# Performance work log

Measured on AMD Instinct MI355X. Metric: run time of the kernel, lower is better.

## Reference

```python
import jax, jax.numpy as jnp
import numpy as np

N, E, F, UNITS, K = 50000, 500000, 128, 256, 3


def setup_inputs() -> dict:
    key = jax.random.key(0)
    k1, k2, k3 = jax.random.split(key, 3)
    x = jax.random.normal(k1, (N, F), dtype=jnp.float32)
    edge_index = jax.random.randint(k2, (2, E), 0, N)
    edge_weight = jnp.ones((E,), dtype=jnp.float32)
    kernel = jax.random.normal(k3, (F * (K + 1), UNITS), dtype=jnp.float32) * 0.02
    bias = jnp.zeros((UNITS,), dtype=jnp.float32)
    return {"x": x, "edge_index": edge_index, "edge_weight": edge_weight,
            "kernel": kernel, "bias": bias}


def _gcn_norm_edge(edge_index, edge_weight, num_nodes):
    # renorm=False, improved=False (tf_geometric gcn_norm_edge):
    # symmetric-normalize original edges, THEN append self-loops with weight 1.0
    row, col = edge_index[0], edge_index[1]
    deg = jax.ops.segment_sum(edge_weight, row, num_segments=num_nodes)
    deg_inv_sqrt = jnp.where(deg > 0, 1.0 / jnp.sqrt(jnp.maximum(deg, 1e-12)), 0.0)
    w = deg_inv_sqrt[row] * edge_weight * deg_inv_sqrt[col]
    loop = jnp.arange(num_nodes)
    row = jnp.concatenate([row, loop])
    col = jnp.concatenate([col, loop])
    w = jnp.concatenate([w, jnp.ones((num_nodes,), dtype=w.dtype)])
    return row, col, w


def reference(x, edge_index, edge_weight, kernel, bias):
    n = x.shape[0]
    row, col, w = _gcn_norm_edge(edge_index, edge_weight, n)
    xs = [x]
    for _ in range(K):
        # out[col] += x[row] * w  (gather -> weight -> scatter-sum)
        h = jax.ops.segment_sum(xs[-1][row] * w[:, None], col, num_segments=n)
        xs.append(h)
    h = jnp.concatenate(xs, axis=-1)  # [N, F*(K+1)]
    out = h @ kernel + bias           # [N, UNITS]
    return out
```

## Files before the change

### kernel.cpp

```cpp
#include <hip/hip_runtime.h>

constexpr int NN = 50000;
constexpr int EE = 500000;
constexpr int FF = 128;
constexpr int UU = 256;
constexpr int KK = 512;
constexpr int NB = (NN + 255) / 256;

using bf16x8 = __attribute__((ext_vector_type(8))) short;
using f32x4  = __attribute__((ext_vector_type(4))) float;

__device__ inline float bf2f(unsigned short b) {
    unsigned u = (unsigned)b << 16; float f; __builtin_memcpy(&f, &u, 4); return f;
}
__device__ inline unsigned short f2bf(float f) {
    unsigned u; __builtin_memcpy(&u, &f, 4);
    u = u + 0x7fffu + ((u >> 16) & 1u);
    return (unsigned short)(u >> 16);
}

typedef __attribute__((address_space(1))) const void GASV;
typedef __attribute__((address_space(3))) void LASV;
__device__ inline void gload_lds16(const void* g, void* l) {
    __builtin_amdgcn_global_load_lds((GASV*)g, (LASV*)l, 16, 0, 0);
}


__global__ __launch_bounds__(256) void k_degcnt(const int* __restrict__ row,
                                                const int* __restrict__ col,
                                                const float* __restrict__ ew,
                                                float* __restrict__ deg,
                                                int* __restrict__ cnt, int E) {
    int e = blockIdx.x * 256 + threadIdx.x;
    if (e < E) {
        atomicAdd(&deg[row[e]], ew[e]);
        atomicAdd(&cnt[col[e]], 1);
    }
}


__global__ __launch_bounds__(256) void k_scan1(const int* __restrict__ cnt,
                                               int* __restrict__ offs,
                                               int* __restrict__ bsum,
                                               float* __restrict__ deg) {
    const int t = threadIdx.x;
    const int gid = blockIdx.x * 256 + t;
    if (gid < NN) {
        float d = deg[gid];
        deg[gid] = (d > 0.f) ? (1.0f / sqrtf(fmaxf(d, 1e-12f))) : 0.f;
    }
    int v = (gid < NN) ? cnt[gid] : 0;
    __shared__ int ts[256];
    ts[t] = v; __syncthreads();
    for (int d = 1; d < 256; d <<= 1) {
        int a = ts[t]; int b = (t >= d) ? ts[t - d] : 0;
        __syncthreads(); ts[t] = a + b; __syncthreads();
    }
    if (gid < NN) offs[gid] = ts[t] - v;
    if (t == 255) bsum[blockIdx.x] = ts[255];
}

__global__ __launch_bounds__(256) void k_scan2(int* __restrict__ bsum) {
    const int t = threadIdx.x;
    int v = (t < NB) ? bsum[t] : 0;
    __shared__ int ts[256];
    ts[t] = v; __syncthreads();
    for (int d = 1; d < 256; d <<= 1) {
        int a = ts[t]; int b = (t >= d) ? ts[t - d] : 0;
        __syncthreads(); ts[t] = a + b; __syncthreads();
    }
    if (t < NB) bsum[t] = ts[t] - v;
}

__global__ __launch_bounds__(256) void k_scan3(int* __restrict__ offs,
                                               int* __restrict__ cursor,
                                               const int* __restrict__ bsum) {
    const int gid = blockIdx.x * 256 + threadIdx.x;
    if (gid < NN) {
        int val = offs[gid] + bsum[blockIdx.x];
        offs[gid] = val;
        cursor[gid] = val;
    }
    if (gid == 0) offs[NN] = EE;
}


__global__ __launch_bounds__(256) void k_scatter(const int* __restrict__ row,
                                                 const int* __restrict__ col,
                                                 const float* __restrict__ ew,
                                                 const float* __restrict__ dis,
                                                 int* __restrict__ cursor,
                                                 int* __restrict__ rows_s,
                                                 float* __restrict__ w_s, int E) {
    int e = blockIdx.x * 256 + threadIdx.x;
    if (e < E) {
        int r = row[e], c = col[e];
        int slot = atomicAdd(&cursor[c], 1);
        rows_s[slot] = r;
        w_s[slot] = dis[r] * ew[e] * dis[c];
    }
}


__global__ __launch_bounds__(256) void k_xcast(const float4* __restrict__ x4,
                                               unsigned short* __restrict__ H) {
    int i = blockIdx.x * 256 + threadIdx.x;
    if (i < NN * 32) {
        int n = i >> 5, c4 = i & 31;
        float4 v = x4[i];
        ushort4 o;
        o.x = f2bf(v.x); o.y = f2bf(v.y); o.z = f2bf(v.z); o.w = f2bf(v.w);
        *reinterpret_cast<ushort4*>(H + (size_t)n * KK + c4 * 4) = o;
    }
}

__global__ __launch_bounds__(256) void k_wcast(const float* __restrict__ W,
                                               unsigned short* __restrict__ Wt) {
    int t = blockIdx.x * 256 + threadIdx.x;
    if (t < KK * UU) {
        int k = t >> 8, c = t & 255;
        Wt[(size_t)c * KK + k] = f2bf(W[t]);
    }
}


__global__ __launch_bounds__(256) void k_prop(const int* __restrict__ offs,
                                              const int* __restrict__ rows_s,
                                              const float* __restrict__ w_s,
                                              unsigned short* __restrict__ H,
                                              int sin, int sout) {
    int wid = (blockIdx.x * 256 + threadIdx.x) >> 6;
    int lane = threadIdx.x & 63;
    if (wid >= NN) return;
    const unsigned short* bin = H + (size_t)sin * FF;
    unsigned self = *reinterpret_cast<const unsigned*>(bin + (size_t)wid * KK + lane * 2);
    float a0 = bf2f((unsigned short)self);
    float a1 = bf2f((unsigned short)(self >> 16));
    const int beg = offs[wid], end = offs[wid + 1];
    int e = beg;
    for (; e + 4 <= end; e += 4) {
        int r0 = rows_s[e], r1 = rows_s[e + 1], r2 = rows_s[e + 2], r3 = rows_s[e + 3];
        float w0 = w_s[e], w1 = w_s[e + 1], w2 = w_s[e + 2], w3 = w_s[e + 3];
        unsigned v0 = *reinterpret_cast<const unsigned*>(bin + (size_t)r0 * KK + lane * 2);
        unsigned v1 = *reinterpret_cast<const unsigned*>(bin + (size_t)r1 * KK + lane * 2);
        unsigned v2 = *reinterpret_cast<const unsigned*>(bin + (size_t)r2 * KK + lane * 2);
        unsigned v3 = *reinterpret_cast<const unsigned*>(bin + (size_t)r3 * KK + lane * 2);
        a0 += bf2f((unsigned short)v0) * w0 + bf2f((unsigned short)v1) * w1
            + bf2f((unsigned short)v2) * w2 + bf2f((unsigned short)v3) * w3;
        a1 += bf2f((unsigned short)(v0 >> 16)) * w0 + bf2f((unsigned short)(v1 >> 16)) * w1
            + bf2f((unsigned short)(v2 >> 16)) * w2 + bf2f((unsigned short)(v3 >> 16)) * w3;
    }
    for (; e < end; ++e) {
        int r = rows_s[e];
        float wv = w_s[e];
        unsigned v = *reinterpret_cast<const unsigned*>(bin + (size_t)r * KK + lane * 2);
        a0 += bf2f((unsigned short)v) * wv;
        a1 += bf2f((unsigned short)(v >> 16)) * wv;
    }
    unsigned o = (unsigned)f2bf(a0) | ((unsigned)f2bf(a1) << 16);
    *reinterpret_cast<unsigned*>(H + (size_t)sout * FF + (size_t)wid * KK + lane * 2) = o;
}


__global__ __launch_bounds__(256, 2) void k_gemm(const unsigned short* __restrict__ H,
                                                 const unsigned short* __restrict__ Wt,
                                                 const float* __restrict__ bias,
                                                 float* __restrict__ out) {
    __shared__ __align__(16) char As[2][128 * 128];
    __shared__ __align__(16) char Bs[2][128 * 128];
    const int t = threadIdx.x;
    const int lane = t & 63;
    const int wv = t >> 6;
    const int wm = wv >> 1;
    const int wn = wv & 1;
    const int brow = (blockIdx.x >> 1) * 128;
    const int bcol = (blockIdx.x & 1) * 128;

    const int r8  = lane >> 3;
    const int b16 = (lane & 7) * 16;

    f32x4 acc[4][4] = {};

    auto stage = [&](int buf, int ks) {
#pragma unroll
        for (int i = 0; i < 8; ++i) {
            int c = wv * 8 + i;
            if (c < 16) {
                int r = c * 8 + r8;
                int gr = brow + r; if (gr >= NN) gr = NN - 1;
                const char* src = (const char*)H + (size_t)gr * (KK * 2) + ks * 128
                                  + (b16 ^ ((r & 7) << 4));
                gload_lds16(src, &As[buf][c * 1024]);
            } else {
                int cc = (c - 16) * 8 + r8;
                int gc = bcol + cc;
                const char* src = (const char*)Wt + (size_t)gc * (KK * 2) + ks * 128
                                  + (b16 ^ ((cc & 7) << 4));
                gload_lds16(src, &Bs[buf][(c - 16) * 1024]);
            }
        }
    };

    auto compute = [&](int buf) {
        bf16x8 af[2][4], bfr[2][4];
#pragma unroll
        for (int kk = 0; kk < 2; ++kk) {
#pragma unroll
            for (int f = 0; f < 4; ++f) {
                int r = wm * 64 + f * 16 + (lane & 15);
                int ba = (kk * 64 + (lane >> 4) * 16) ^ ((r & 7) << 4);
                af[kk][f] = *reinterpret_cast<const bf16x8*>(&As[buf][r * 128 + ba]);
                int cc = wn * 64 + f * 16 + (lane & 15);
                int bb = (kk * 64 + (lane >> 4) * 16) ^ ((cc & 7) << 4);
                bfr[kk][f] = *reinterpret_cast<const bf16x8*>(&Bs[buf][cc * 128 + bb]);
            }
        }
#pragma unroll
        for (int kk = 0; kk < 2; ++kk)
#pragma unroll
            for (int fm = 0; fm < 4; ++fm)
#pragma unroll
                for (int fn = 0; fn < 4; ++fn)
                    acc[fm][fn] = __builtin_amdgcn_mfma_f32_16x16x32_bf16(
                        af[kk][fm], bfr[kk][fn], acc[fm][fn], 0, 0, 0);
    };

    stage(0, 0);
    __syncthreads();
    for (int ks = 0; ks < 8; ++ks) {
        if (ks < 7) stage((ks + 1) & 1, ks + 1);
        compute(ks & 1);
        __syncthreads();
    }

#pragma unroll
    for (int fn = 0; fn < 4; ++fn) {
        int col = bcol + wn * 64 + fn * 16 + (lane & 15);
        float bs = bias[col];
#pragma unroll
        for (int fm = 0; fm < 4; ++fm) {
#pragma unroll
            for (int r4 = 0; r4 < 4; ++r4) {
                int grow = brow + wm * 64 + fm * 16 + (lane >> 4) * 4 + r4;
                if (grow < NN)
                    out[(size_t)grow * UU + col] = acc[fm][fn][r4] + bs;
            }
        }
    }
}


extern "C" void kernel_launch(void* const* d_in, const int* in_sizes, int n_in,
                              void* d_out, int out_size, void* d_ws, size_t ws_size,
                              hipStream_t stream) {
    const float* x    = (const float*)d_in[0];
    const int*   ei   = (const int*)d_in[1];
    const float* ew   = (const float*)d_in[2];
    const float* Wk   = (const float*)d_in[3];
    const float* bias = (const float*)d_in[4];
    float* out = (float*)d_out;

    const int* row = ei;
    const int* col = ei + EE;

    char* ws = (char*)d_ws;
    size_t off = 0;
    auto alloc = [&](size_t bytes) {
        size_t o = off;
        off += (bytes + 255) & ~(size_t)255;
        return o;
    };
    float*          deg    = (float*)(ws + alloc((size_t)NN * sizeof(float)));
    int*            cnt    = (int*)  (ws + alloc((size_t)NN * sizeof(int)));
    int*            cursor = (int*)  (ws + alloc((size_t)NN * sizeof(int)));
    int*            offs   = (int*)  (ws + alloc((size_t)(NN + 1) * sizeof(int)));
    int*            bsum   = (int*)  (ws + alloc((size_t)256 * sizeof(int)));
    int*            rows_s = (int*)  (ws + alloc((size_t)EE * sizeof(int)));
    float*          w_s    = (float*)(ws + alloc((size_t)EE * sizeof(float)));
    unsigned short* Hcat   = (unsigned short*)(ws + alloc((size_t)NN * KK * sizeof(short)));
    unsigned short* Wt     = (unsigned short*)(ws + alloc((size_t)KK * UU * sizeof(short)));

    const int geb = (EE + 255) / 256;

    hipMemsetAsync(deg, 0, (size_t)NN * sizeof(float), stream);
    hipMemsetAsync(cnt, 0, (size_t)NN * sizeof(int), stream);
    k_degcnt<<<geb, 256, 0, stream>>>(row, col, ew, deg, cnt, EE);
    k_scan1<<<NB, 256, 0, stream>>>(cnt, offs, bsum, deg);
    k_scan2<<<1, 256, 0, stream>>>(bsum);
    k_scan3<<<NB, 256, 0, stream>>>(offs, cursor, bsum);
    k_scatter<<<geb, 256, 0, stream>>>(row, col, ew, deg, cursor, rows_s, w_s, EE);

    k_xcast<<<(NN * 32 + 255) / 256, 256, 0, stream>>>((const float4*)x, Hcat);
    k_wcast<<<(KK * UU + 255) / 256, 256, 0, stream>>>(Wk, Wt);

    const int gprop = (NN * 64 + 255) / 256;
    k_prop<<<gprop, 256, 0, stream>>>(offs, rows_s, w_s, Hcat, 0, 1);
    k_prop<<<gprop, 256, 0, stream>>>(offs, rows_s, w_s, Hcat, 1, 2);
    k_prop<<<gprop, 256, 0, stream>>>(offs, rows_s, w_s, Hcat, 2, 3);

    k_gemm<<<391 * 2, 256, 0, stream>>>(Hcat, Wt, bias, out);
}
```

Before: 303.3 us.

## Fuse setup kernels, pack edge data, and split wavefront across edges in propagation

Folds the x-to-bf16 cast into the degree/count kernel and the weight transpose-cast into the scatter kernel, which cuts the launch count. Packs each edge's row index and normalized weight into one uint2, so propagation does a single 8-byte load per edge. Propagation now splits each wavefront into four groups of 16 lanes; each group handles a different edge with 16-byte feature loads, and the partial sums are combined with cross-lane shuffles. This gives more memory-level parallelism per wavefront, at the cost of extra shuffles and more register pressure.

```diff
diff --git a/kernel.cpp b/kernel.cpp
--- a/kernel.cpp
+++ b/kernel.cpp
@@ -26,15 +26,27 @@
 }
 
 
-__global__ __launch_bounds__(256) void k_degcnt(const int* __restrict__ row,
-                                                const int* __restrict__ col,
-                                                const float* __restrict__ ew,
-                                                float* __restrict__ deg,
-                                                int* __restrict__ cnt, int E) {
-    int e = blockIdx.x * 256 + threadIdx.x;
-    if (e < E) {
-        atomicAdd(&deg[row[e]], ew[e]);
-        atomicAdd(&cnt[col[e]], 1);
+__global__ __launch_bounds__(256) void k_deg_x(const int* __restrict__ row,
+                                               const int* __restrict__ col,
+                                               const float* __restrict__ ew,
+                                               float* __restrict__ deg,
+                                               int* __restrict__ cnt,
+                                               const float4* __restrict__ x4,
+                                               unsigned short* __restrict__ H) {
+    const int i = blockIdx.x * 256 + threadIdx.x;
+    if (i < NN * 32) {
+        int n = i >> 5, c4 = i & 31;
+        float4 v = x4[i];
+        ushort4 o;
+        o.x = f2bf(v.x); o.y = f2bf(v.y); o.z = f2bf(v.z); o.w = f2bf(v.w);
+        *reinterpret_cast<ushort4*>(H + (size_t)n * KK + c4 * 4) = o;
+    }
+    if (blockIdx.x % 3 == 0) {
+        int e = (blockIdx.x / 3) * 256 + threadIdx.x;
+        if (e < EE) {
+            atomicAdd(&deg[row[e]], ew[e]);
+            atomicAdd(&cnt[col[e]], 1);
+        }
     }
 }
 
@@ -90,75 +102,85 @@
                                                  const float* __restrict__ ew,
                                                  const float* __restrict__ dis,
                                                  int* __restrict__ cursor,
-                                                 int* __restrict__ rows_s,
-                                                 float* __restrict__ w_s, int E) {
-    int e = blockIdx.x * 256 + threadIdx.x;
-    if (e < E) {
+                                                 uint2* __restrict__ edata,
+                                                 const float* __restrict__ W,
+                                                 unsigned short* __restrict__ Wt) {
+    const int e = blockIdx.x * 256 + threadIdx.x;
+    if (e < EE) {
         int r = row[e], c = col[e];
         int slot = atomicAdd(&cursor[c], 1);
-        rows_s[slot] = r;
-        w_s[slot] = dis[r] * ew[e] * dis[c];
-    }
-}
-
-
-__global__ __launch_bounds__(256) void k_xcast(const float4* __restrict__ x4,
-                                               unsigned short* __restrict__ H) {
-    int i = blockIdx.x * 256 + threadIdx.x;
-    if (i < NN * 32) {
-        int n = i >> 5, c4 = i & 31;
-        float4 v = x4[i];
-        ushort4 o;
-        o.x = f2bf(v.x); o.y = f2bf(v.y); o.z = f2bf(v.z); o.w = f2bf(v.w);
-        *reinterpret_cast<ushort4*>(H + (size_t)n * KK + c4 * 4) = o;
-    }
-}
-
-__global__ __launch_bounds__(256) void k_wcast(const float* __restrict__ W,
-                                               unsigned short* __restrict__ Wt) {
-    int t = blockIdx.x * 256 + threadIdx.x;
-    if (t < KK * UU) {
-        int k = t >> 8, c = t & 255;
-        Wt[(size_t)c * KK + k] = f2bf(W[t]);
+        float wv = dis[r] * ew[e] * dis[c];
+        uint2 d; d.x = (unsigned)r; __builtin_memcpy(&d.y, &wv, 4);
+        edata[slot] = d;
+    }
+    if (e < KK * UU) {
+        int k = e >> 8, c = e & 255;
+        Wt[(size_t)c * KK + k] = f2bf(W[e]);
     }
 }
 
 
 __global__ __launch_bounds__(256) void k_prop(const int* __restrict__ offs,
-                                              const int* __restrict__ rows_s,
-                                              const float* __restrict__ w_s,
+                                              const uint2* __restrict__ edata,
                                               unsigned short* __restrict__ H,
                                               int sin, int sout) {
-    int wid = (blockIdx.x * 256 + threadIdx.x) >> 6;
-    int lane = threadIdx.x & 63;
-    if (wid >= NN) return;
+    const int wid = (blockIdx.x * 256 + threadIdx.x) >> 6;
+    const int lane = threadIdx.x & 63;
+    const int g = lane >> 4;
+    const int sl = lane & 15;
+
     const unsigned short* bin = H + (size_t)sin * FF;
-    unsigned self = *reinterpret_cast<const unsigned*>(bin + (size_t)wid * KK + lane * 2);
-    float a0 = bf2f((unsigned short)self);
-    float a1 = bf2f((unsigned short)(self >> 16));
+    const unsigned short* rowp = bin + (size_t)wid * KK + sl * 8;
+
+    float a[8];
+    {
+        uint4 s4 = *reinterpret_cast<const uint4*>(rowp);
+        const unsigned sw[4] = {s4.x, s4.y, s4.z, s4.w};
+#pragma unroll
+        for (int j = 0; j < 8; ++j) {
+            float v = bf2f((unsigned short)(sw[j >> 1] >> ((j & 1) * 16)));
+            a[j] = (g == 0) ? v : 0.f;
+        }
+    }
+
     const int beg = offs[wid], end = offs[wid + 1];
-    int e = beg;
-    for (; e + 4 <= end; e += 4) {
-        int r0 = rows_s[e], r1 = rows_s[e + 1], r2 = rows_s[e + 2], r3 = rows_s[e + 3];
-        float w0 = w_s[e], w1 = w_s[e + 1], w2 = w_s[e + 2], w3 = w_s[e + 3];
-        unsigned v0 = *reinterpret_cast<const unsigned*>(bin + (size_t)r0 * KK + lane * 2);
-        unsigned v1 = *reinterpret_cast<const unsigned*>(bin + (size_t)r1 * KK + lane * 2);
-        unsigned v2 = *reinterpret_cast<const unsigned*>(bin + (size_t)r2 * KK + lane * 2);
-        unsigned v3 = *reinterpret_cast<const unsigned*>(bin + (size_t)r3 * KK + lane * 2);
-        a0 += bf2f((unsigned short)v0) * w0 + bf2f((unsigned short)v1) * w1
-            + bf2f((unsigned short)v2) * w2 + bf2f((unsigned short)v3) * w3;
-        a1 += bf2f((unsigned short)(v0 >> 16)) * w0 + bf2f((unsigned short)(v1 >> 16)) * w1
-            + bf2f((unsigned short)(v2 >> 16)) * w2 + bf2f((unsigned short)(v3 >> 16)) * w3;
-    }
-    for (; e < end; ++e) {
-        int r = rows_s[e];
-        float wv = w_s[e];
-        unsigned v = *reinterpret_cast<const unsigned*>(bin + (size_t)r * KK + lane * 2);
-        a0 += bf2f((unsigned short)v) * wv;
-        a1 += bf2f((unsigned short)(v >> 16)) * wv;
-    }
-    unsigned o = (unsigned)f2bf(a0) | ((unsigned)f2bf(a1) << 16);
-    *reinterpret_cast<unsigned*>(H + (size_t)sout * FF + (size_t)wid * KK + lane * 2) = o;
+    int e = beg + g;
+    for (; e + 4 < end; e += 8) {
+        uint2 d0 = edata[e], d1 = edata[e + 4];
+        float w0, w1; __builtin_memcpy(&w0, &d0.y, 4); __builtin_memcpy(&w1, &d1.y, 4);
+        uint4 v0 = *reinterpret_cast<const uint4*>(bin + (size_t)d0.x * KK + sl * 8);
+        uint4 v1 = *reinterpret_cast<const uint4*>(bin + (size_t)d1.x * KK + sl * 8);
+        const unsigned u0[4] = {v0.x, v0.y, v0.z, v0.w};
+        const unsigned u1[4] = {v1.x, v1.y, v1.z, v1.w};
+#pragma unroll
+        for (int j = 0; j < 8; ++j)
+            a[j] += bf2f((unsigned short)(u0[j >> 1] >> ((j & 1) * 16))) * w0
+                  + bf2f((unsigned short)(u1[j >> 1] >> ((j & 1) * 16))) * w1;
+    }
+    if (e < end) {
+        uint2 d0 = edata[e];
+        float w0; __builtin_memcpy(&w0, &d0.y, 4);
+        uint4 v0 = *reinterpret_cast<const uint4*>(bin + (size_t)d0.x * KK + sl * 8);
+        const unsigned u0[4] = {v0.x, v0.y, v0.z, v0.w};
+#pragma unroll
+        for (int j = 0; j < 8; ++j)
+            a[j] += bf2f((unsigned short)(u0[j >> 1] >> ((j & 1) * 16))) * w0;
+    }
+
+#pragma unroll
+    for (int j = 0; j < 8; ++j) {
+        a[j] += __shfl_xor(a[j], 16);
+        a[j] += __shfl_xor(a[j], 32);
+    }
+
+    if (lane < 16) {
+        uint4 o;
+        o.x = (unsigned)f2bf(a[0]) | ((unsigned)f2bf(a[1]) << 16);
+        o.y = (unsigned)f2bf(a[2]) | ((unsigned)f2bf(a[3]) << 16);
+        o.z = (unsigned)f2bf(a[4]) | ((unsigned)f2bf(a[5]) << 16);
+        o.w = (unsigned)f2bf(a[6]) | ((unsigned)f2bf(a[7]) << 16);
+        *reinterpret_cast<uint4*>(H + (size_t)sout * FF + (size_t)wid * KK + sl * 8) = o;
+    }
 }
 
 
@@ -275,28 +297,25 @@
     int*            cursor = (int*)  (ws + alloc((size_t)NN * sizeof(int)));
     int*            offs   = (int*)  (ws + alloc((size_t)(NN + 1) * sizeof(int)));
     int*            bsum   = (int*)  (ws + alloc((size_t)256 * sizeof(int)));
-    int*            rows_s = (int*)  (ws + alloc((size_t)EE * sizeof(int)));
-    float*          w_s    = (float*)(ws + alloc((size_t)EE * sizeof(float)));
+    uint2*          edata  = (uint2*)(ws + alloc((size_t)EE * sizeof(uint2)));
     unsigned short* Hcat   = (unsigned short*)(ws + alloc((size_t)NN * KK * sizeof(short)));
     unsigned short* Wt     = (unsigned short*)(ws + alloc((size_t)KK * UU * sizeof(short)));
 
-    const int geb = (EE + 255) / 256;
-
     hipMemsetAsync(deg, 0, (size_t)NN * sizeof(float), stream);
     hipMemsetAsync(cnt, 0, (size_t)NN * sizeof(int), stream);
-    k_degcnt<<<geb, 256, 0, stream>>>(row, col, ew, deg, cnt, EE);
+
+    k_deg_x<<<(NN * 32 + 255) / 256, 256, 0, stream>>>(row, col, ew, deg, cnt,
+                                                       (const float4*)x, Hcat);
     k_scan1<<<NB, 256, 0, stream>>>(cnt, offs, bsum, deg);
     k_scan2<<<1, 256, 0, stream>>>(bsum);
     k_scan3<<<NB, 256, 0, stream>>>(offs, cursor, bsum);
-    k_scatter<<<geb, 256, 0, stream>>>(row, col, ew, deg, cursor, rows_s, w_s, EE);
-
-    k_xcast<<<(NN * 32 + 255) / 256, 256, 0, stream>>>((const float4*)x, Hcat);
-    k_wcast<<<(KK * UU + 255) / 256, 256, 0, stream>>>(Wk, Wt);
-
-    const int gprop = (NN * 64 + 255) / 256;
-    k_prop<<<gprop, 256, 0, stream>>>(offs, rows_s, w_s, Hcat, 0, 1);
-    k_prop<<<gprop, 256, 0, stream>>>(offs, rows_s, w_s, Hcat, 1, 2);
-    k_prop<<<gprop, 256, 0, stream>>>(offs, rows_s, w_s, Hcat, 2, 3);
+    k_scatter<<<(EE + 255) / 256, 256, 0, stream>>>(row, col, ew, deg, cursor,
+                                                    edata, Wk, Wt);
+
+    const int gprop = NN / 4;
+    k_prop<<<gprop, 256, 0, stream>>>(offs, edata, Hcat, 0, 1);
+    k_prop<<<gprop, 256, 0, stream>>>(offs, edata, Hcat, 1, 2);
+    k_prop<<<gprop, 256, 0, stream>>>(offs, edata, Hcat, 2, 3);
 
     k_gemm<<<391 * 2, 256, 0, stream>>>(Hcat, Wt, bias, out);
 }
```

Result: faster. 277.0 us (-8.7%).
